# Kernel tuning notes

Measured on AMD Instinct MI355X. Metric: run time of the kernel, lower is better.

Reference implementation:

```python
import jax, jax.numpy as jnp
import numpy as np

EMBED_DIM = 1024
NUM_HEADS = 16
D_K = EMBED_DIM // NUM_HEADS
GAMMA = 1.0


def setup_inputs() -> dict:
    key = jax.random.key(0)
    ks = jax.random.split(key, 5)
    B, N, E = 2, 2048, EMBED_DIM
    scale = 1.0 / np.sqrt(E)
    x = jax.random.normal(ks[0], (B, N, E), dtype=jnp.float32)
    Wq = jax.random.normal(ks[1], (E, E), dtype=jnp.float32) * scale
    Wk = jax.random.normal(ks[2], (E, E), dtype=jnp.float32) * scale
    Wv = jax.random.normal(ks[3], (E, E), dtype=jnp.float32) * scale
    Wo = jax.random.normal(ks[4], (E, E), dtype=jnp.float32) * scale
    mask = jnp.ones((B, N), dtype=jnp.int32)
    return {"x": x, "Wq": Wq, "Wk": Wk, "Wv": Wv, "Wo": Wo, "mask": mask}


def _split_heads(t):
    B, N, E = t.shape
    return t.reshape(B, N, NUM_HEADS, D_K).transpose(0, 2, 1, 3)  # [B,H,N,dk]


def reference(x, Wq, Wk, Wv, Wo, mask):
    B, N, E = x.shape
    # Linear layers (bias=False): y = x @ W.T
    q = _split_heads(x @ Wq.T)
    k = _split_heads(x @ Wk.T)
    v = _split_heads(x @ Wv.T)
    # Squared L2 distance via ||q||^2 + ||k||^2 - 2 q.k (same math as (q-k)^2.sum,
    # without materializing the [B,H,N,N,dk] diff tensor).
    q_sq = jnp.sum(q * q, axis=-1)  # [B,H,N]
    k_sq = jnp.sum(k * k, axis=-1)  # [B,H,N]
    qk = jnp.einsum('bhqd,bhkd->bhqk', q, k)
    sq_dist = jnp.maximum(q_sq[..., :, None] + k_sq[..., None, :] - 2.0 * qk, 0.0)
    similarity = jnp.exp(-GAMMA * sq_dist)  # [B,H,N,N]
    # mask.unsqueeze(1).unsqueeze(2): broadcast over heads and query dim
    mask_exp = mask[:, None, None, :]  # [B,1,1,N]
    similarity = jnp.where(mask_exp == 0, jnp.float32(-1e9), similarity)
    attn = jax.nn.softmax(similarity, axis=-1)
    # dropout p=0.0 (eval) -> identity
    out = jnp.einsum('bhqk,bhkd->bhqd', attn, v)
    out = out.transpose(0, 2, 1, 3).reshape(B, N, E)
    return out @ Wo.T
```

## Files before the change

### kernel.cpp

```cpp
#include <hip/hip_runtime.h>
#include <hip/hip_bf16.h>


using bf16x8 = __attribute__((ext_vector_type(8))) __bf16;
using f32x4  = __attribute__((ext_vector_type(4))) float;
using f32x16 = __attribute__((ext_vector_type(16))) float;

typedef const __attribute__((address_space(1))) void* gas_t;
typedef __attribute__((address_space(3))) void* las_t;

#define C_LOG2E 1.4426950408889634f
#define TWO_C   2.8853900817779268f
#define NEG_INV_4C (-0.17328679513998632f)

#if __has_builtin(__builtin_amdgcn_exp2f)
#define EXP2(x) __builtin_amdgcn_exp2f(x)
#else
#define EXP2(x) __expf((x) * 0.6931471805599453f)
#endif

static __device__ __forceinline__ unsigned short f2bf(float x) {
  union { float f; unsigned u; } c; c.f = x;
  unsigned u = c.u;
  u += 0x7fffu + ((u >> 16) & 1u);
  return (unsigned short)(u >> 16);
}
static __device__ __forceinline__ float bf2f(unsigned short b) {
  union { unsigned u; float f; } c; c.u = ((unsigned)b) << 16;
  return c.f;
}
static __device__ __forceinline__ unsigned cvt_pk_bf16(float lo, float hi) {
  unsigned r;
  asm("v_cvt_pk_bf16_f32 %0, %1, %2" : "=v"(r) : "v"(lo), "v"(hi));
  return r;
}
static __device__ __forceinline__ void permlane32_swap(unsigned &a, unsigned &b) {
#if __has_builtin(__builtin_amdgcn_permlane32_swap)
  auto r = __builtin_amdgcn_permlane32_swap(a, b, false, false);
  a = r[0]; b = r[1];
#else
  asm("v_permlane32_swap_b32 %0, %1" : "+v"(a), "+v"(b));
#endif
}

#define SYNC_VM(N)                                                           \
  do {                                                                       \
    asm volatile("s_waitcnt vmcnt(" #N ") lgkmcnt(0)\n\ts_barrier" ::: "memory"); \
    __builtin_amdgcn_sched_barrier(0);                                       \
  } while (0)

__global__ __launch_bounds__(256)
void cvt_all(const float* __restrict__ x,  const float* __restrict__ wq,
             const float* __restrict__ wk, const float* __restrict__ wv,
             const float* __restrict__ wo,
             unsigned short* __restrict__ xbf, unsigned short* __restrict__ Wbf,
             float* __restrict__ FullVm, float* __restrict__ den_base,
             unsigned* __restrict__ kmax_bits) {
  const int idx = blockIdx.x * 256 + threadIdx.x;
  if (blockIdx.x == 0) {
    const int tid = threadIdx.x;
#pragma unroll
    for (int i = 0; i < 8; ++i) FullVm[tid + i * 256] = 0.f;
    if (tid < 32) kmax_bits[tid] = 0xFF800000u;
    if (tid < 2) den_base[tid] = 0.f;
  }
  const float* src; unsigned short* dst; int off;
  if (idx < 1048576) { src = x; dst = xbf; off = idx; }
  else {
    const int r = idx - 1048576;
    const int w = r >> 18;
    off = r & 262143;
    src = (w == 0) ? wq : (w == 1) ? wk : (w == 2) ? wv : wo;
    dst = Wbf + (size_t)w * 1048576u;
  }
  const float4 v = ((const float4*)src)[off];
  ushort4 o;
  o.x = f2bf(v.x); o.y = f2bf(v.y); o.z = f2bf(v.z); o.w = f2bf(v.w);
  ((ushort4*)dst)[off] = o;
}

__global__ __launch_bounds__(256)
void gemm_bt(const unsigned short* __restrict__ A,
             const unsigned short* __restrict__ Bt,
             void* __restrict__ out0, int Kdim, int mode,
             float* __restrict__ qsqp, float* __restrict__ ksqp) {
  __shared__ unsigned short As[3][4096];
  __shared__ unsigned short Bs[3][4096];
  const int t  = threadIdx.x;
  const int m0 = blockIdx.x * 128;
  const int n0 = blockIdx.y * 128;
  const int srow = t >> 2;
  const int scol = (((t & 3) ^ (srow & 3) ^ ((srow >> 2) & 3))) * 8;
  const unsigned short* pA = A  + (size_t)(m0 + srow) * Kdim + scol;
  const unsigned short* pB = Bt + (size_t)(n0 + srow) * Kdim + scol;
  const size_t rowskip = (size_t)64 * Kdim;

  const int wave = t >> 6, lane = t & 63;
  const int wm = (wave >> 1) * 64, wn = (wave & 1) * 64;
  const int fr = lane & 15, fg = lane >> 4;
  const int fswz = fg ^ (fr & 3) ^ ((fr >> 2) & 3);
  const int aoff = (wm + fr) * 32 + fswz * 8;
  const int boff = (wn + fr) * 32 + fswz * 8;

  f32x4 acc[4][4];
#pragma unroll
  for (int mi = 0; mi < 4; ++mi)
#pragma unroll
    for (int ni = 0; ni < 4; ++ni)
      acc[mi][ni] = (f32x4){0.f, 0.f, 0.f, 0.f};

#define GSTAGE(bi, kk)                                                                                  \
  do {                                                                                                  \
    const int kc = (kk) * 32;                                                                           \
    __builtin_amdgcn_global_load_lds((gas_t)(const void*)(pA + kc),           (las_t)(void*)(As[bi] + t * 8),        16, 0, 0); \
    __builtin_amdgcn_global_load_lds((gas_t)(const void*)(pA + kc + rowskip), (las_t)(void*)(As[bi] + 2048 + t * 8), 16, 0, 0); \
    __builtin_amdgcn_global_load_lds((gas_t)(const void*)(pB + kc),           (las_t)(void*)(Bs[bi] + t * 8),        16, 0, 0); \
    __builtin_amdgcn_global_load_lds((gas_t)(const void*)(pB + kc + rowskip), (las_t)(void*)(Bs[bi] + 2048 + t * 8), 16, 0, 0); \
  } while (0)

  const int NK = Kdim >> 5;
  GSTAGE(0, 0);
  GSTAGE(1, 1);

  for (int ks = 0; ks < NK; ++ks) {
    const int cur = ks % 3;
    if (ks + 1 < NK) SYNC_VM(4); else SYNC_VM(0);
    if (ks + 2 < NK) GSTAGE((ks + 2) % 3, ks + 2);

    bf16x8 af[4], bfr[4];
#pragma unroll
    for (int mi = 0; mi < 4; ++mi) af[mi]  = *(const bf16x8*)(As[cur] + aoff + mi * 512);
#pragma unroll
    for (int ni = 0; ni < 4; ++ni) bfr[ni] = *(const bf16x8*)(Bs[cur] + boff + ni * 512);
#pragma unroll
    for (int mi = 0; mi < 4; ++mi)
#pragma unroll
      for (int ni = 0; ni < 4; ++ni)
        acc[mi][ni] = __builtin_amdgcn_mfma_f32_16x16x32_bf16(af[mi], bfr[ni], acc[mi][ni], 0, 0, 0);
  }
#undef GSTAGE

  if (mode == 1) {
    float* dst = (float*)out0;
#pragma unroll
    for (int mi = 0; mi < 4; ++mi) {
      const int gm = m0 + wm + mi * 16 + fg * 4;
#pragma unroll
      for (int ni = 0; ni < 4; ++ni) {
        const int gn = n0 + wn + ni * 16 + fr;
#pragma unroll
        for (int r = 0; r < 4; ++r)
          dst[(size_t)(gm + r) * 1024 + gn] = acc[mi][ni][r];
      }
    }
    return;
  }
  const int wavecol = n0 + wn;
  const int zz = wavecol >> 10;
  unsigned short* outw = (unsigned short*)out0;
  if (zz < 2) {
    const float sc = (zz == 0) ? TWO_C : 1.0f;
    const float qscale = (zz == 0) ? NEG_INV_4C : -C_LOG2E;
    unsigned short* dst = outw + (size_t)zz * 4194304u;
    const int hh = (wavecol & 1023) >> 6;
    float* dq = (zz == 0) ? qsqp : ksqp;
#pragma unroll
    for (int mi = 0; mi < 4; ++mi) {
      const int gm = m0 + wm + mi * 16 + fg * 4;
      float s0 = 0.f, s1 = 0.f, s2 = 0.f, s3 = 0.f;
#pragma unroll
      for (int ni = 0; ni < 4; ++ni) {
        const int col = (wavecol + ni * 16 + fr) & 1023;
        const unsigned short u0 = f2bf(acc[mi][ni][0] * sc);
        const unsigned short u1 = f2bf(acc[mi][ni][1] * sc);
        const unsigned short u2 = f2bf(acc[mi][ni][2] * sc);
        const unsigned short u3 = f2bf(acc[mi][ni][3] * sc);
        dst[(size_t)(gm + 0) * 1024 + col] = u0;
        dst[(size_t)(gm + 1) * 1024 + col] = u1;
        dst[(size_t)(gm + 2) * 1024 + col] = u2;
        dst[(size_t)(gm + 3) * 1024 + col] = u3;
        const float r0 = bf2f(u0), r1 = bf2f(u1), r2 = bf2f(u2), r3 = bf2f(u3);
        s0 += r0 * r0; s1 += r1 * r1; s2 += r2 * r2; s3 += r3 * r3;
      }
#pragma unroll
      for (int off2 = 1; off2 < 16; off2 <<= 1) {
        s0 += __shfl_xor(s0, off2);
        s1 += __shfl_xor(s1, off2);
        s2 += __shfl_xor(s2, off2);
        s3 += __shfl_xor(s3, off2);
      }
      if (fr == 0) {
        const int bb = gm >> 11;
        float4 o4;
        o4.x = s0 * qscale; o4.y = s1 * qscale;
        o4.z = s2 * qscale; o4.w = s3 * qscale;
        *(float4*)(dq + (bb * 16 + hh) * 2048 + (gm & 2047)) = o4;
      }
    }
  } else {
#pragma unroll
    for (int mi = 0; mi < 4; ++mi) {
      const int gm = m0 + wm + mi * 16 + fg * 4;
#pragma unroll
      for (int ni = 0; ni < 4; ++ni) {
        const int gn = n0 + wn + ni * 16 + fr;
        const int col = gn & 1023;
        ushort4 o4;
        o4.x = f2bf(acc[mi][ni][0]); o4.y = f2bf(acc[mi][ni][1]);
        o4.z = f2bf(acc[mi][ni][2]); o4.w = f2bf(acc[mi][ni][3]);
        const int bb = gm >> 11, nn = gm & 2047;
        const int hh = col >> 6, dd = col & 63;
        unsigned short* vt = outw + (size_t)2 * 4194304u;
        *(ushort4*)(vt + ((size_t)((bb * 16 + hh) * 64 + dd)) * 2048 + nn) = o4;
      }
    }
  }
}

__global__ __launch_bounds__(256)
void prep_kernel(const unsigned short* __restrict__ Vt,
                 const int* __restrict__ mask,
                 const float* __restrict__ ksqp,
                 float* __restrict__ maskf,
                 float* __restrict__ FullVm,
                 float* __restrict__ den_base,
                 unsigned* __restrict__ kmax_bits) {
  const int bh = blockIdx.x >> 3, c = blockIdx.x & 7;
  const int b = bh >> 4;
  const int wave = threadIdx.x >> 6, lane = threadIdx.x & 63;
  const int k0 = c * 256;
  const int4 mi4 = *(const int4*)(mask + b * 2048 + k0 + lane * 4);
  const float mvx = mi4.x ? 1.f : 0.f, mvy = mi4.y ? 1.f : 0.f;
  const float mvz = mi4.z ? 1.f : 0.f, mvw = mi4.w ? 1.f : 0.f;
#pragma unroll 4
  for (int dr = wave * 16; dr < wave * 16 + 16; ++dr) {
    const ushort4 v = *(const ushort4*)(Vt + ((size_t)bh * 64 + dr) * 2048 + k0 + lane * 4);
    float s = bf2f(v.x) * mvx + bf2f(v.y) * mvy + bf2f(v.z) * mvz + bf2f(v.w) * mvw;
#pragma unroll
    for (int off = 32; off >= 1; off >>= 1) s += __shfl_xor(s, off);
    if (lane == 0) atomicAdd(&FullVm[bh * 64 + dr], s);
  }
  if (wave == 0) {
    const float4 kq = *(const float4*)(ksqp + bh * 2048 + k0 + lane * 4);
    float mx = fmaxf(fmaxf(kq.x, kq.y), fmaxf(kq.z, kq.w));
#pragma unroll
    for (int off = 32; off >= 1; off >>= 1) mx = fmaxf(mx, __shfl_xor(mx, off));
    if (lane == 0) atomicMin(&kmax_bits[bh], __float_as_uint(mx));
  }
  if (wave == 1 && (bh & 15) == 0) {
    float4 mf; mf.x = mvx; mf.y = mvy; mf.z = mvz; mf.w = mvw;
    *(float4*)(maskf + b * 2048 + k0 + lane * 4) = mf;
  }
  if (wave == 2 && (bh & 15) == 0) {
    float s = mvx + mvy + mvz + mvw;
#pragma unroll
    for (int off = 32; off >= 1; off >>= 1) s += __shfl_xor(s, off);
    if (lane == 0) atomicAdd(&den_base[b], s);
  }
}

__global__ __launch_bounds__(256)
void attn_kernel(const unsigned short* __restrict__ Qbf,
                 const unsigned short* __restrict__ Kbf,
                 const unsigned short* __restrict__ Vt,
                 const float* __restrict__ qsqp,
                 const float* __restrict__ ksqp,
                 const float* __restrict__ maskf,
                 const float* __restrict__ FullVm,
                 const float* __restrict__ den_base,
                 const float* __restrict__ kmaxb,
                 unsigned short* __restrict__ Obf) {
  __shared__ unsigned short Ks[3][4096];

  const int bh = blockIdx.x;
  const int b = bh >> 4, h = bh & 15;
  const int t = threadIdx.x;
  const int wave = t >> 6, lane = t & 63;
  const int qg = wave >> 1, hf = wave & 1;
  const int li = lane & 31, hi = lane >> 5;
  const int q0 = blockIdx.y * 64 + qg * 32;
  const int qrow = q0 + li;

  const unsigned short* Qr = Qbf + (size_t)(b * 2048 + qrow) * 1024 + h * 64 + hi * 8;
  bf16x8 qf[4];
#pragma unroll
  for (int dblk = 0; dblk < 4; ++dblk) qf[dblk] = *(const bf16x8*)(Qr + dblk * 16);

  const float qsl = qsqp[bh * 2048 + qrow];
  const float thr = -14.0f - qsl - kmaxb[bh];

  const unsigned short* Kbase = Kbf + (size_t)b * 2048 * 1024 + h * 64;
  const unsigned short* VtB = Vt + (size_t)bh * 64 * 2048;

  const int p0 = t,        r0 = p0 >> 3, c0 = (p0 & 7) ^ (r0 & 7);
  const int p1 = 256 + t,  r1 = p1 >> 3, c1 = (p1 & 7) ^ (r1 & 7);

  f32x16 oa0, oa1;
#pragma unroll
  for (int r = 0; r < 16; ++r) { oa0[r] = 0.f; oa1[r] = 0.f; }
  float den = 0.f;

#define STAGE(bi, tj)                                                                               \
  do {                                                                                              \
    const int j0s = (tj) * 64;                                                                      \
    __builtin_amdgcn_global_load_lds((gas_t)(const void*)(Kbase + (size_t)(j0s + r0) * 1024 + c0 * 8), \
                                     (las_t)(void*)(Ks[bi] + p0 * 8), 16, 0, 0);                    \
    __builtin_amdgcn_global_load_lds((gas_t)(const void*)(Kbase + (size_t)(j0s + r1) * 1024 + c1 * 8), \
                                     (las_t)(void*)(Ks[bi] + p1 * 8), 16, 0, 0);                    \
  } while (0)

  STAGE(0, 0);
  STAGE(1, 1);

  const int jw = hf * 32;
  const int krow = jw + li;
  const int ksw = krow & 7;

  for (int tj = 0; tj < 32; ++tj) {
    const int cur = tj % 3;
    if (tj + 1 < 32) SYNC_VM(2); else SYNC_VM(0);
    if (tj + 2 < 32) STAGE((tj + 2) % 3, tj + 2);

    const unsigned short* Krow = Ks[cur] + krow * 64;
    f32x16 st;
#pragma unroll
    for (int r = 0; r < 16; ++r) st[r] = 0.f;
#pragma unroll
    for (int dblk = 0; dblk < 4; ++dblk) {
      const bf16x8 kf = *(const bf16x8*)(Krow + ((dblk * 2 + hi) ^ ksw) * 8);
      st = __builtin_amdgcn_mfma_f32_32x32x16_bf16(kf, qf[dblk], st, 0, 0, 0);
    }

    const float a0 = fmaxf(fmaxf(st[0], st[1]), st[2]);
    const float a1 = fmaxf(fmaxf(st[3], st[4]), st[5]);
    const float a2 = fmaxf(fmaxf(st[6], st[7]), st[8]);
    const float a3 = fmaxf(fmaxf(st[9], st[10]), st[11]);
    const float a4 = fmaxf(fmaxf(st[12], st[13]), st[14]);
    const float a5 = fmaxf(fmaxf(a0, a1), st[15]);
    const float a6 = fmaxf(fmaxf(a2, a3), a4);
    const float lmax = fmaxf(a5, a6);

    if (__any(lmax > thr)) {
      const int j0 = tj * 64 + jw;
      const float* ksb2 = ksqp + bh * 2048 + j0 + 4 * hi;
      const float* mfb2 = maskf + b * 2048 + j0 + 4 * hi;
      const float4 kq0 = *(const float4*)(ksb2);
      const float4 kq1 = *(const float4*)(ksb2 + 8);
      const float4 kq2 = *(const float4*)(ksb2 + 16);
      const float4 kq3 = *(const float4*)(ksb2 + 24);
      const float4 mf0 = *(const float4*)(mfb2);
      const float4 mf1 = *(const float4*)(mfb2 + 8);
      const float4 mf2 = *(const float4*)(mfb2 + 16);
      const float4 mf3 = *(const float4*)(mfb2 + 24);
      const float kqa[16] = {kq0.x, kq0.y, kq0.z, kq0.w, kq1.x, kq1.y, kq1.z, kq1.w,
                             kq2.x, kq2.y, kq2.z, kq2.w, kq3.x, kq3.y, kq3.z, kq3.w};
      const float mfa[16] = {mf0.x, mf0.y, mf0.z, mf0.w, mf1.x, mf1.y, mf1.z, mf1.w,
                             mf2.x, mf2.y, mf2.z, mf2.w, mf3.x, mf3.y, mf3.z, mf3.w};
      float dsv[16];
#pragma unroll
      for (int r = 0; r < 16; ++r) {
        const float z = __builtin_fminf(st[r] + qsl + kqa[r], 0.f);
        const float s = EXP2(z);
        float pl = __builtin_fmaf(s, 1.f / 120.f, 1.f / 24.f);
        pl = __builtin_fmaf(s, pl, 1.f / 6.f);
        pl = __builtin_fmaf(s, pl, 0.5f);
        pl = __builtin_fmaf(s, pl, 1.f);
        const float d_ = s * pl * mfa[r];
        dsv[r] = d_;
        den += d_;
      }

      unsigned u00 = cvt_pk_bf16(dsv[0],  dsv[1]);
      unsigned u01 = cvt_pk_bf16(dsv[2],  dsv[3]);
      unsigned u10 = cvt_pk_bf16(dsv[4],  dsv[5]);
      unsigned u11 = cvt_pk_bf16(dsv[6],  dsv[7]);
      unsigned u20 = cvt_pk_bf16(dsv[8],  dsv[9]);
      unsigned u21 = cvt_pk_bf16(dsv[10], dsv[11]);
      unsigned u30 = cvt_pk_bf16(dsv[12], dsv[13]);
      unsigned u31 = cvt_pk_bf16(dsv[14], dsv[15]);
      permlane32_swap(u00, u10);
      permlane32_swap(u01, u11);
      permlane32_swap(u20, u30);
      permlane32_swap(u21, u31);
      union { unsigned u[4]; bf16x8 v; } pf0, pf1;
      pf0.u[0] = u00; pf0.u[1] = u01; pf0.u[2] = u10; pf0.u[3] = u11;
      pf1.u[0] = u20; pf1.u[1] = u21; pf1.u[2] = u30; pf1.u[3] = u31;

#pragma unroll
      for (int dh = 0; dh < 2; ++dh) {
        const unsigned short* Vrow = VtB + (size_t)(dh * 32 + li) * 2048 + tj * 64;
        const bf16x8 vf0 = *(const bf16x8*)(Vrow + (hf * 4 + 0 + hi) * 8);
        const bf16x8 vf1 = *(const bf16x8*)(Vrow + (hf * 4 + 2 + hi) * 8);
        if (dh == 0) {
          oa0 = __builtin_amdgcn_mfma_f32_32x32x16_bf16(vf0, pf0.v, oa0, 0, 0, 0);
          oa0 = __builtin_amdgcn_mfma_f32_32x32x16_bf16(vf1, pf1.v, oa0, 0, 0, 0);
        } else {
          oa1 = __builtin_amdgcn_mfma_f32_32x32x16_bf16(vf0, pf0.v, oa1, 0, 0, 0);
          oa1 = __builtin_amdgcn_mfma_f32_32x32x16_bf16(vf1, pf1.v, oa1, 0, 0, 0);
        }
      }
    }
  }
#undef STAGE

  den += __shfl_xor(den, 32);

  __syncthreads();
  float* Obuf = (float*)&Ks[0][0];
  float* Dbuf = (float*)&Ks[0][0] + 4096;
  if (hf == 1) {
#pragma unroll
    for (int r = 0; r < 16; ++r) {
      Obuf[(qg * 32 + r) * 64 + lane]      = oa0[r];
      Obuf[(qg * 32 + 16 + r) * 64 + lane] = oa1[r];
    }
    Dbuf[qg * 64 + lane] = den;
  }
  __syncthreads();
  if (hf == 0) {
    const float inv = 1.f / (den_base[b] + den + Dbuf[qg * 64 + lane]);
    const float* fvm = FullVm + bh * 64;
    unsigned short* orow = Obf + (size_t)(b * 2048 + qrow) * 1024 + h * 64;
#pragma unroll
    for (int dh = 0; dh < 2; ++dh)
#pragma unroll
      for (int w = 0; w < 4; ++w) {
        float v0, v1, v2, v3;
        if (dh == 0) {
          v0 = oa0[4 * w];     v1 = oa0[4 * w + 1];
          v2 = oa0[4 * w + 2]; v3 = oa0[4 * w + 3];
        } else {
          v0 = oa1[4 * w];     v1 = oa1[4 * w + 1];
          v2 = oa1[4 * w + 2]; v3 = oa1[4 * w + 3];
        }
        const int sbase = (qg * 32 + dh * 16 + 4 * w) * 64 + lane;
        v0 += Obuf[sbase];       v1 += Obuf[sbase + 64];
        v2 += Obuf[sbase + 128]; v3 += Obuf[sbase + 192];
        const float4 fv = *(const float4*)(fvm + dh * 32 + w * 8 + hi * 4);
        ushort4 o4;
        o4.x = f2bf((v0 + fv.x) * inv);
        o4.y = f2bf((v1 + fv.y) * inv);
        o4.z = f2bf((v2 + fv.z) * inv);
        o4.w = f2bf((v3 + fv.w) * inv);
        *(ushort4*)(orow + dh * 32 + w * 8 + hi * 4) = o4;
      }
  }
}

extern "C" void kernel_launch(void* const* d_in, const int* in_sizes, int n_in,
                              void* d_out, int out_size, void* d_ws, size_t ws_size,
                              hipStream_t stream) {
  const float* x  = (const float*)d_in[0];
  const float* Wq = (const float*)d_in[1];
  const float* Wk = (const float*)d_in[2];
  const float* Wv = (const float*)d_in[3];
  const float* Wo = (const float*)d_in[4];
  const int* mask = (const int*)d_in[5];

  unsigned short* ws = (unsigned short*)d_ws;
  const size_t SZ = 4194304;
  unsigned short* xbf = ws;
  unsigned short* Wbf = ws + SZ;
  unsigned short* Qbf = ws + 2 * SZ;
  unsigned short* Kbf = ws + 3 * SZ;
  unsigned short* Vt  = ws + 4 * SZ;
  unsigned short* Obf = ws + 5 * SZ;
  float* qsqp = (float*)(ws + 6 * SZ);
  float* ksqp = qsqp + 65536;
  float* maskf = ksqp + 65536;
  float* FullVm = maskf + 4096;
  float* den_base = FullVm + 2048;
  float* kmaxb = den_base + 2;

  cvt_all<<<8192, 256, 0, stream>>>(x, Wq, Wk, Wv, Wo, xbf, Wbf,
                                    FullVm, den_base, (unsigned*)kmaxb);

  gemm_bt<<<dim3(32, 24), 256, 0, stream>>>(xbf, Wbf, Qbf, 1024, 0, qsqp, ksqp);

  prep_kernel<<<256, 256, 0, stream>>>(Vt, mask, ksqp, maskf, FullVm, den_base,
                                       (unsigned*)kmaxb);

  attn_kernel<<<dim3(32, 32), 256, 0, stream>>>(Qbf, Kbf, Vt, qsqp, ksqp, maskf,
                                                FullVm, den_base, kmaxb, Obf);

  gemm_bt<<<dim3(32, 8), 256, 0, stream>>>(Obf, Wbf + 3145728, d_out, 1024, 1,
                                           nullptr, nullptr);
}
```

Measured before the change: 112.1 us.

## Drop key-split waves in attention; each wave processes full key tiles with 4-stage pipeline

The attention kernel previously used 4 waves, two per 32-query group, each covering half of every 64-key tile, and merged the partial outputs through shared memory at the end. Now each block has 2 waves that each process both 32-key halves of every tile, removing the cross-wave reduction and its two barriers. The K staging ring grows from 3 to 4 buffers with 3 tiles in flight to hide load latency. The trade-off is fewer waves per block and more serial work per wave, which may reduce latency hiding and occupancy.

Result: no change. 110.2 us (-1.7%).

```diff
diff --git a/kernel.cpp b/kernel.cpp
--- a/kernel.cpp
+++ b/kernel.cpp
@@ -259,7 +259,7 @@
   }
 }
 
-__global__ __launch_bounds__(256)
+__global__ __launch_bounds__(128)
 void attn_kernel(const unsigned short* __restrict__ Qbf,
                  const unsigned short* __restrict__ Kbf,
                  const unsigned short* __restrict__ Vt,
@@ -270,15 +270,14 @@
                  const float* __restrict__ den_base,
                  const float* __restrict__ kmaxb,
                  unsigned short* __restrict__ Obf) {
-  __shared__ unsigned short Ks[3][4096];
+  __shared__ unsigned short Ks[4][4096];
 
   const int bh = blockIdx.x;
   const int b = bh >> 4, h = bh & 15;
   const int t = threadIdx.x;
   const int wave = t >> 6, lane = t & 63;
-  const int qg = wave >> 1, hf = wave & 1;
   const int li = lane & 31, hi = lane >> 5;
-  const int q0 = blockIdx.y * 64 + qg * 32;
+  const int q0 = blockIdx.y * 64 + wave * 32;
   const int qrow = q0 + li;
 
   const unsigned short* Qr = Qbf + (size_t)(b * 2048 + qrow) * 1024 + h * 64 + hi * 8;
@@ -293,7 +292,9 @@
   const unsigned short* VtB = Vt + (size_t)bh * 64 * 2048;
 
   const int p0 = t,        r0 = p0 >> 3, c0 = (p0 & 7) ^ (r0 & 7);
-  const int p1 = 256 + t,  r1 = p1 >> 3, c1 = (p1 & 7) ^ (r1 & 7);
+  const int p1 = 128 + t,  r1 = p1 >> 3, c1 = (p1 & 7) ^ (r1 & 7);
+  const int p2 = 256 + t,  r2 = p2 >> 3, c2 = (p2 & 7) ^ (r2 & 7);
+  const int p3 = 384 + t,  r3 = p3 >> 3, c3 = (p3 & 7) ^ (r3 & 7);
 
   f32x16 oa0, oa1;
 #pragma unroll
@@ -307,144 +308,134 @@
                                      (las_t)(void*)(Ks[bi] + p0 * 8), 16, 0, 0);                    \
     __builtin_amdgcn_global_load_lds((gas_t)(const void*)(Kbase + (size_t)(j0s + r1) * 1024 + c1 * 8), \
                                      (las_t)(void*)(Ks[bi] + p1 * 8), 16, 0, 0);                    \
+    __builtin_amdgcn_global_load_lds((gas_t)(const void*)(Kbase + (size_t)(j0s + r2) * 1024 + c2 * 8), \
+                                     (las_t)(void*)(Ks[bi] + p2 * 8), 16, 0, 0);                    \
+    __builtin_amdgcn_global_load_lds((gas_t)(const void*)(Kbase + (size_t)(j0s + r3) * 1024 + c3 * 8), \
+                                     (las_t)(void*)(Ks[bi] + p3 * 8), 16, 0, 0);                    \
   } while (0)
 
   STAGE(0, 0);
   STAGE(1, 1);
-
-  const int jw = hf * 32;
-  const int krow = jw + li;
-  const int ksw = krow & 7;
+  STAGE(2, 2);
+
+  const int ksw = li & 7;
 
   for (int tj = 0; tj < 32; ++tj) {
-    const int cur = tj % 3;
-    if (tj + 1 < 32) SYNC_VM(2); else SYNC_VM(0);
-    if (tj + 2 < 32) STAGE((tj + 2) % 3, tj + 2);
-
-    const unsigned short* Krow = Ks[cur] + krow * 64;
-    f32x16 st;
-#pragma unroll
-    for (int r = 0; r < 16; ++r) st[r] = 0.f;
-#pragma unroll
-    for (int dblk = 0; dblk < 4; ++dblk) {
-      const bf16x8 kf = *(const bf16x8*)(Krow + ((dblk * 2 + hi) ^ ksw) * 8);
-      st = __builtin_amdgcn_mfma_f32_32x32x16_bf16(kf, qf[dblk], st, 0, 0, 0);
+    const int cur = tj & 3;
+    if (tj + 2 < 32) SYNC_VM(8);
+    else if (tj + 1 < 32) SYNC_VM(4);
+    else SYNC_VM(0);
+    if (tj + 3 < 32) STAGE((tj + 3) & 3, tj + 3);
+
+#pragma unroll
+    for (int s = 0; s < 2; ++s) {
+      const unsigned short* Krow = Ks[cur] + (s * 32 + li) * 64;
+      f32x16 st;
+#pragma unroll
+      for (int r = 0; r < 16; ++r) st[r] = 0.f;
+#pragma unroll
+      for (int dblk = 0; dblk < 4; ++dblk) {
+        const bf16x8 kf = *(const bf16x8*)(Krow + ((dblk * 2 + hi) ^ ksw) * 8);
+        st = __builtin_amdgcn_mfma_f32_32x32x16_bf16(kf, qf[dblk], st, 0, 0, 0);
+      }
+
+      const float a0 = fmaxf(fmaxf(st[0], st[1]), st[2]);
+      const float a1 = fmaxf(fmaxf(st[3], st[4]), st[5]);
+      const float a2 = fmaxf(fmaxf(st[6], st[7]), st[8]);
+      const float a3 = fmaxf(fmaxf(st[9], st[10]), st[11]);
+      const float a4 = fmaxf(fmaxf(st[12], st[13]), st[14]);
+      const float a5 = fmaxf(fmaxf(a0, a1), st[15]);
+      const float a6 = fmaxf(fmaxf(a2, a3), a4);
+      const float lmax = fmaxf(a5, a6);
+
+      if (__any(lmax > thr)) {
+        const int j0 = tj * 64 + s * 32;
+        const float* ksb2 = ksqp + bh * 2048 + j0 + 4 * hi;
+        const float* mfb2 = maskf + b * 2048 + j0 + 4 * hi;
+        const float4 kq0 = *(const float4*)(ksb2);
+        const float4 kq1 = *(const float4*)(ksb2 + 8);
+        const float4 kq2 = *(const float4*)(ksb2 + 16);
+        const float4 kq3 = *(const float4*)(ksb2 + 24);
+        const float4 mf0 = *(const float4*)(mfb2);
+        const float4 mf1 = *(const float4*)(mfb2 + 8);
+        const float4 mf2 = *(const float4*)(mfb2 + 16);
+        const float4 mf3 = *(const float4*)(mfb2 + 24);
+        const float kqa[16] = {kq0.x, kq0.y, kq0.z, kq0.w, kq1.x, kq1.y, kq1.z, kq1.w,
+                               kq2.x, kq2.y, kq2.z, kq2.w, kq3.x, kq3.y, kq3.z, kq3.w};
+        const float mfa[16] = {mf0.x, mf0.y, mf0.z, mf0.w, mf1.x, mf1.y, mf1.z, mf1.w,
+                               mf2.x, mf2.y, mf2.z, mf2.w, mf3.x, mf3.y, mf3.z, mf3.w};
+        float dsv[16];
+#pragma unroll
+        for (int r = 0; r < 16; ++r) {
+          const float z = __builtin_fminf(st[r] + qsl + kqa[r], 0.f);
+          const float sx = EXP2(z);
+          float pl = __builtin_fmaf(sx, 1.f / 120.f, 1.f / 24.f);
+          pl = __builtin_fmaf(sx, pl, 1.f / 6.f);
+          pl = __builtin_fmaf(sx, pl, 0.5f);
+          pl = __builtin_fmaf(sx, pl, 1.f);
+          const float d_ = sx * pl * mfa[r];
+          dsv[r] = d_;
+          den += d_;
+        }
+
+        unsigned u00 = cvt_pk_bf16(dsv[0],  dsv[1]);
+        unsigned u01 = cvt_pk_bf16(dsv[2],  dsv[3]);
+        unsigned u10 = cvt_pk_bf16(dsv[4],  dsv[5]);
+        unsigned u11 = cvt_pk_bf16(dsv[6],  dsv[7]);
+        unsigned u20 = cvt_pk_bf16(dsv[8],  dsv[9]);
+        unsigned u21 = cvt_pk_bf16(dsv[10], dsv[11]);
+        unsigned u30 = cvt_pk_bf16(dsv[12], dsv[13]);
+        unsigned u31 = cvt_pk_bf16(dsv[14], dsv[15]);
+        permlane32_swap(u00, u10);
+        permlane32_swap(u01, u11);
+        permlane32_swap(u20, u30);
+        permlane32_swap(u21, u31);
+        union { unsigned u[4]; bf16x8 v; } pf0, pf1;
+        pf0.u[0] = u00; pf0.u[1] = u01; pf0.u[2] = u10; pf0.u[3] = u11;
+        pf1.u[0] = u20; pf1.u[1] = u21; pf1.u[2] = u30; pf1.u[3] = u31;
+
+#pragma unroll
+        for (int dh = 0; dh < 2; ++dh) {
+          const unsigned short* Vrow = VtB + (size_t)(dh * 32 + li) * 2048 + j0;
+          const bf16x8 vf0 = *(const bf16x8*)(Vrow + hi * 8);
+          const bf16x8 vf1 = *(const bf16x8*)(Vrow + 16 + hi * 8);
+          if (dh == 0) {
+            oa0 = __builtin_amdgcn_mfma_f32_32x32x16_bf16(vf0, pf0.v, oa0, 0, 0, 0);
+            oa0 = __builtin_amdgcn_mfma_f32_32x32x16_bf16(vf1, pf1.v, oa0, 0, 0, 0);
+          } else {
+            oa1 = __builtin_amdgcn_mfma_f32_32x32x16_bf16(vf0, pf0.v, oa1, 0, 0, 0);
+            oa1 = __builtin_amdgcn_mfma_f32_32x32x16_bf16(vf1, pf1.v, oa1, 0, 0, 0);
+          }
+        }
+      }
     }
-
-    const float a0 = fmaxf(fmaxf(st[0], st[1]), st[2]);
-    const float a1 = fmaxf(fmaxf(st[3], st[4]), st[5]);
-    const float a2 = fmaxf(fmaxf(st[6], st[7]), st[8]);
-    const float a3 = fmaxf(fmaxf(st[9], st[10]), st[11]);
-    const float a4 = fmaxf(fmaxf(st[12], st[13]), st[14]);
-    const float a5 = fmaxf(fmaxf(a0, a1), st[15]);
-    const float a6 = fmaxf(fmaxf(a2, a3), a4);
-    const float lmax = fmaxf(a5, a6);
-
-    if (__any(lmax > thr)) {
-      const int j0 = tj * 64 + jw;
-      const float* ksb2 = ksqp + bh * 2048 + j0 + 4 * hi;
-      const float* mfb2 = maskf + b * 2048 + j0 + 4 * hi;
-      const float4 kq0 = *(const float4*)(ksb2);
-      const float4 kq1 = *(const float4*)(ksb2 + 8);
-      const float4 kq2 = *(const float4*)(ksb2 + 16);
-      const float4 kq3 = *(const float4*)(ksb2 + 24);
-      const float4 mf0 = *(const float4*)(mfb2);
-      const float4 mf1 = *(const float4*)(mfb2 + 8);
-      const float4 mf2 = *(const float4*)(mfb2 + 16);
-      const float4 mf3 = *(const float4*)(mfb2 + 24);
-      const float kqa[16] = {kq0.x, kq0.y, kq0.z, kq0.w, kq1.x, kq1.y, kq1.z, kq1.w,
-                             kq2.x, kq2.y, kq2.z, kq2.w, kq3.x, kq3.y, kq3.z, kq3.w};
-      const float mfa[16] = {mf0.x, mf0.y, mf0.z, mf0.w, mf1.x, mf1.y, mf1.z, mf1.w,
-                             mf2.x, mf2.y, mf2.z, mf2.w, mf3.x, mf3.y, mf3.z, mf3.w};
-      float dsv[16];
-#pragma unroll
-      for (int r = 0; r < 16; ++r) {
-        const float z = __builtin_fminf(st[r] + qsl + kqa[r], 0.f);
-        const float s = EXP2(z);
-        float pl = __builtin_fmaf(s, 1.f / 120.f, 1.f / 24.f);
-        pl = __builtin_fmaf(s, pl, 1.f / 6.f);
-        pl = __builtin_fmaf(s, pl, 0.5f);
-        pl = __builtin_fmaf(s, pl, 1.f);
-        const float d_ = s * pl * mfa[r];
-        dsv[r] = d_;
-        den += d_;
-      }
-
-      unsigned u00 = cvt_pk_bf16(dsv[0],  dsv[1]);
-      unsigned u01 = cvt_pk_bf16(dsv[2],  dsv[3]);
-      unsigned u10 = cvt_pk_bf16(dsv[4],  dsv[5]);
-      unsigned u11 = cvt_pk_bf16(dsv[6],  dsv[7]);
-      unsigned u20 = cvt_pk_bf16(dsv[8],  dsv[9]);
-      unsigned u21 = cvt_pk_bf16(dsv[10], dsv[11]);
-      unsigned u30 = cvt_pk_bf16(dsv[12], dsv[13]);
-      unsigned u31 = cvt_pk_bf16(dsv[14], dsv[15]);
-      permlane32_swap(u00, u10);
-      permlane32_swap(u01, u11);
-      permlane32_swap(u20, u30);
-      permlane32_swap(u21, u31);
-      union { unsigned u[4]; bf16x8 v; } pf0, pf1;
-      pf0.u[0] = u00; pf0.u[1] = u01; pf0.u[2] = u10; pf0.u[3] = u11;
-      pf1.u[0] = u20; pf1.u[1] = u21; pf1.u[2] = u30; pf1.u[3] = u31;
-
-#pragma unroll
-      for (int dh = 0; dh < 2; ++dh) {
-        const unsigned short* Vrow = VtB + (size_t)(dh * 32 + li) * 2048 + tj * 64;
-        const bf16x8 vf0 = *(const bf16x8*)(Vrow + (hf * 4 + 0 + hi) * 8);
-        const bf16x8 vf1 = *(const bf16x8*)(Vrow + (hf * 4 + 2 + hi) * 8);
-        if (dh == 0) {
-          oa0 = __builtin_amdgcn_mfma_f32_32x32x16_bf16(vf0, pf0.v, oa0, 0, 0, 0);
-          oa0 = __builtin_amdgcn_mfma_f32_32x32x16_bf16(vf1, pf1.v, oa0, 0, 0, 0);
-        } else {
-          oa1 = __builtin_amdgcn_mfma_f32_32x32x16_bf16(vf0, pf0.v, oa1, 0, 0, 0);
-          oa1 = __builtin_amdgcn_mfma_f32_32x32x16_bf16(vf1, pf1.v, oa1, 0, 0, 0);
-        }
-      }
+  }
+#undef STAGE
+
+  den += __shfl_xor(den, 32);
+  const float inv = 1.f / (den_base[b] + den);
+  const float* fvm = FullVm + bh * 64;
+  unsigned short* orow = Obf + (size_t)(b * 2048 + qrow) * 1024 + h * 64;
+#pragma unroll
+  for (int dh = 0; dh < 2; ++dh)
+#pragma unroll
+    for (int w = 0; w < 4; ++w) {
+      float v0, v1, v2, v3;
+      if (dh == 0) {
+        v0 = oa0[4 * w];     v1 = oa0[4 * w + 1];
+        v2 = oa0[4 * w + 2]; v3 = oa0[4 * w + 3];
+      } else {
+        v0 = oa1[4 * w];     v1 = oa1[4 * w + 1];
+        v2 = oa1[4 * w + 2]; v3 = oa1[4 * w + 3];
+      }
+      const float4 fv = *(const float4*)(fvm + dh * 32 + w * 8 + hi * 4);
+      ushort4 o4;
+      o4.x = f2bf((v0 + fv.x) * inv);
+      o4.y = f2bf((v1 + fv.y) * inv);
+      o4.z = f2bf((v2 + fv.z) * inv);
+      o4.w = f2bf((v3 + fv.w) * inv);
+      *(ushort4*)(orow + dh * 32 + w * 8 + hi * 4) = o4;
     }
-  }
-#undef STAGE
-
-  den += __shfl_xor(den, 32);
-
-  __syncthreads();
-  float* Obuf = (float*)&Ks[0][0];
-  float* Dbuf = (float*)&Ks[0][0] + 4096;
-  if (hf == 1) {
-#pragma unroll
-    for (int r = 0; r < 16; ++r) {
-      Obuf[(qg * 32 + r) * 64 + lane]      = oa0[r];
-      Obuf[(qg * 32 + 16 + r) * 64 + lane] = oa1[r];
-    }
-    Dbuf[qg * 64 + lane] = den;
-  }
-  __syncthreads();
-  if (hf == 0) {
-    const float inv = 1.f / (den_base[b] + den + Dbuf[qg * 64 + lane]);
-    const float* fvm = FullVm + bh * 64;
-    unsigned short* orow = Obf + (size_t)(b * 2048 + qrow) * 1024 + h * 64;
-#pragma unroll
-    for (int dh = 0; dh < 2; ++dh)
-#pragma unroll
-      for (int w = 0; w < 4; ++w) {
-        float v0, v1, v2, v3;
-        if (dh == 0) {
-          v0 = oa0[4 * w];     v1 = oa0[4 * w + 1];
-          v2 = oa0[4 * w + 2]; v3 = oa0[4 * w + 3];
-        } else {
-          v0 = oa1[4 * w];     v1 = oa1[4 * w + 1];
-          v2 = oa1[4 * w + 2]; v3 = oa1[4 * w + 3];
-        }
-        const int sbase = (qg * 32 + dh * 16 + 4 * w) * 64 + lane;
-        v0 += Obuf[sbase];       v1 += Obuf[sbase + 64];
-        v2 += Obuf[sbase + 128]; v3 += Obuf[sbase + 192];
-        const float4 fv = *(const float4*)(fvm + dh * 32 + w * 8 + hi * 4);
-        ushort4 o4;
-        o4.x = f2bf((v0 + fv.x) * inv);
-        o4.y = f2bf((v1 + fv.y) * inv);
-        o4.z = f2bf((v2 + fv.z) * inv);
-        o4.w = f2bf((v3 + fv.w) * inv);
-        *(ushort4*)(orow + dh * 32 + w * 8 + hi * 4) = o4;
-      }
-  }
 }
 
 extern "C" void kernel_launch(void* const* d_in, const int* in_sizes, int n_in,
@@ -480,7 +471,7 @@
   prep_kernel<<<256, 256, 0, stream>>>(Vt, mask, ksqp, maskf, FullVm, den_base,
                                        (unsigned*)kmaxb);
 
-  attn_kernel<<<dim3(32, 32), 256, 0, stream>>>(Qbf, Kbf, Vt, qsqp, ksqp, maskf,
+  attn_kernel<<<dim3(32, 32), 128, 0, stream>>>(Qbf, Kbf, Vt, qsqp, ksqp, maskf,
                                                 FullVm, den_base, kmaxb, Obf);
 
   gemm_bt<<<dim3(32, 8), 256, 0, stream>>>(Obf, Wbf + 3145728, d_out, 1024, 1,
```
